# Kernel optimization log

Hardware: AMD Instinct MI355X
Metric: run time of the kernel (lower is better)

## Reference

```python
import jax, jax.numpy as jnp
import numpy as np

K = 256        # top-k positions kept along the sparse (sequence) axis
GROUPS = 16    # number of channel groups
P = 2          # Lp norm order
EPS = 1e-9


def setup_inputs() -> dict:
    key = jax.random.key(0)
    x = jax.random.normal(key, (32, 2048, 1024), dtype=jnp.float32)
    return {"x": x}


def reference(x):
    B, S, C = x.shape              # batch, sparse axis (seq), group axis (channels)
    g = GROUPS
    gs = C // g                    # channels per group
    # group-wise Lp norm: (B, S, g)
    xg = x.reshape(B, S, g, gs)
    norms = jnp.power(jnp.sum(jnp.power(jnp.abs(xg), P), axis=-1) + EPS, 1.0 / P)
    # topk along the sparse axis per (batch, group)
    norms_t = norms.transpose(0, 2, 1).reshape(B * g, S)   # (B*g, S)
    _, idx = jax.lax.top_k(norms_t, K)                      # (B*g, K)
    # scatter binary mask at topk positions
    rows = jnp.arange(B * g, dtype=jnp.int32)[:, None]
    mask = jnp.zeros((B * g, S), dtype=x.dtype).at[rows, idx].set(1.0)
    mask = mask.reshape(B, g, S).transpose(0, 2, 1)         # (B, S, g)
    # broadcast mask over channels within each group and multiply
    out = (mask[:, :, :, None] * xg).reshape(B, S, C)
    return out
```

## Files before the change

### kernel.cpp

```cpp
#include <hip/hip_runtime.h>


#define BB 32
#define SS 2048
#define GG 16
#define KTOP 256

typedef float f32x4 __attribute__((ext_vector_type(4)));

__device__ inline double shfl_xor_dbl(double v, int m) {
  union {
    double d;
    int i[2];
  } u;
  u.d = v;
  u.i[0] = __shfl_xor(u.i[0], m, 64);
  u.i[1] = __shfl_xor(u.i[1], m, 64);
  return u.d;
}

__global__ __launch_bounds__(1024, 8) void gsa_fused3(
    const float4* __restrict__ x4, float4* __restrict__ out4) {
  __shared__ float norm[SS];
  __shared__ unsigned int Tch_sh;
  __shared__ int Tscl_sh;
  const int t = threadIdx.x;
  const int lane16 = t & 15;
  const int srow = t >> 4;
  const int b = blockIdx.x >> 4;
  const int g = blockIdx.x & 15;
  const size_t bbase = (size_t)b * SS;
  const int chunk = g * 16 + lane16;

  for (int it = 0; it < 16; ++it) {
    const int s0 = it * 128 + srow;
    const int s1 = s0 + 64;
    const float4 va = x4[(bbase + s0) * 256 + chunk];
    const float4 vb = x4[(bbase + s1) * 256 + chunk];
    double da = (double)va.x * va.x + (double)va.y * va.y +
                (double)va.z * va.z + (double)va.w * va.w;
    double db = (double)vb.x * vb.x + (double)vb.y * vb.y +
                (double)vb.z * vb.z + (double)vb.w * vb.w;
    da += shfl_xor_dbl(da, 1);
    db += shfl_xor_dbl(db, 1);
    da += shfl_xor_dbl(da, 2);
    db += shfl_xor_dbl(db, 2);
    da += shfl_xor_dbl(da, 4);
    db += shfl_xor_dbl(db, 4);
    da += shfl_xor_dbl(da, 8);
    db += shfl_xor_dbl(db, 8);
    if (lane16 == 0) {
      norm[s0] = sqrtf(__fadd_rn((float)da, 1e-9f));
      norm[s1] = sqrtf(__fadd_rn((float)db, 1e-9f));
    }
  }
  __syncthreads();

  if (t < 64) {
    unsigned int nb[32];
#pragma unroll
    for (int j = 0; j < 32; ++j) nb[j] = __float_as_uint(norm[j * 64 + t]);
    unsigned long long T = 0ULL;
    for (int bit = 41; bit >= 0; --bit) {
      const unsigned long long cand = T | (1ULL << bit);
      const unsigned int ch = (unsigned int)(cand >> 11);
      const int scl = 2047 - (int)(cand & 2047ULL);
      int cnt = 0;
#pragma unroll
      for (int j = 0; j < 32; ++j) {
        const bool pred =
            (nb[j] > ch) | ((nb[j] == ch) & ((t + j * 64) <= scl));
        cnt += (int)__popcll(__ballot(pred));
      }
      if (cnt >= KTOP) T = cand;
    }
    if (t == 0) {
      Tch_sh = (unsigned int)(T >> 11);
      Tscl_sh = 2047 - (int)(T & 2047ULL);
    }
  }
  __syncthreads();
  const unsigned int ch = Tch_sh;
  const int scl = Tscl_sh;

  for (int it = 0; it < 16; ++it) {
    const int s0 = it * 128 + srow;
    const int s1 = s0 + 64;
    const unsigned int n0 = __float_as_uint(norm[s0]);
    const unsigned int n1 = __float_as_uint(norm[s1]);
    const bool sel0 = (n0 > ch) | ((n0 == ch) & (s0 <= scl));
    const bool sel1 = (n1 > ch) | ((n1 == ch) & (s1 <= scl));
    float4 v0 = make_float4(0.f, 0.f, 0.f, 0.f);
    float4 v1 = make_float4(0.f, 0.f, 0.f, 0.f);
    if (sel0) v0 = x4[(bbase + s0) * 256 + chunk];
    if (sel1) v1 = x4[(bbase + s1) * 256 + chunk];
    __builtin_nontemporal_store(*(const f32x4*)&v0,
                                (f32x4*)(out4 + (bbase + s0) * 256 + chunk));
    __builtin_nontemporal_store(*(const f32x4*)&v1,
                                (f32x4*)(out4 + (bbase + s1) * 256 + chunk));
  }
}

extern "C" void kernel_launch(void* const* d_in, const int* in_sizes, int n_in,
                              void* d_out, int out_size, void* d_ws,
                              size_t ws_size, hipStream_t stream) {
  const float4* x4 = (const float4*)d_in[0];
  float4* out4 = (float4*)d_out;
  gsa_fused3<<<BB * GG, 1024, 0, stream>>>(x4, out4);
}
```

Baseline: 473.5 us.

## Remap blocks for L2 reuse, halve block size, use plain stores

Blocks are reordered so that consecutive block IDs cover 8 batches and the same group, rather than all 16 groups of one batch. This changes which blocks run together and whether re-reads of x hit in cache. Block size drops from 1024 to 512 threads with 4 loads in flight per thread in the norm pass. The nontemporal stores become ordinary stores, which may let output writes pollute L2 and evict x before the second pass re-reads it.

After: 504.4 us. 1.07x slower.

```diff
diff --git a/kernel.cpp b/kernel.cpp
--- a/kernel.cpp
+++ b/kernel.cpp
@@ -5,8 +5,6 @@
 #define SS 2048
 #define GG 16
 #define KTOP 256
-
-typedef float f32x4 __attribute__((ext_vector_type(4)));
 
 __device__ inline double shfl_xor_dbl(double v, int m) {
   union {
@@ -19,39 +17,39 @@
   return u.d;
 }
 
-__global__ __launch_bounds__(1024, 8) void gsa_fused3(
-    const float4* __restrict__ x4, float4* __restrict__ out4) {
+__global__ __launch_bounds__(512, 4) void gsa_v4(const float4* __restrict__ x4,
+                                                 float4* __restrict__ out4) {
   __shared__ float norm[SS];
   __shared__ unsigned int Tch_sh;
   __shared__ int Tscl_sh;
   const int t = threadIdx.x;
   const int lane16 = t & 15;
   const int srow = t >> 4;
-  const int b = blockIdx.x >> 4;
-  const int g = blockIdx.x & 15;
+  const int n = blockIdx.x;
+  const int g = (n >> 3) & 15;
+  const int b = ((n >> 7) << 3) | (n & 7);
   const size_t bbase = (size_t)b * SS;
   const int chunk = g * 16 + lane16;
 
   for (int it = 0; it < 16; ++it) {
-    const int s0 = it * 128 + srow;
-    const int s1 = s0 + 64;
-    const float4 va = x4[(bbase + s0) * 256 + chunk];
-    const float4 vb = x4[(bbase + s1) * 256 + chunk];
-    double da = (double)va.x * va.x + (double)va.y * va.y +
-                (double)va.z * va.z + (double)va.w * va.w;
-    double db = (double)vb.x * vb.x + (double)vb.y * vb.y +
-                (double)vb.z * vb.z + (double)vb.w * vb.w;
-    da += shfl_xor_dbl(da, 1);
-    db += shfl_xor_dbl(db, 1);
-    da += shfl_xor_dbl(da, 2);
-    db += shfl_xor_dbl(db, 2);
-    da += shfl_xor_dbl(da, 4);
-    db += shfl_xor_dbl(db, 4);
-    da += shfl_xor_dbl(da, 8);
-    db += shfl_xor_dbl(db, 8);
+    const int sb = it * 128 + srow;
+    float4 v[4];
+#pragma unroll
+    for (int j = 0; j < 4; ++j) v[j] = x4[(bbase + sb + j * 32) * 256 + chunk];
+    double d[4];
+#pragma unroll
+    for (int j = 0; j < 4; ++j)
+      d[j] = (double)v[j].x * v[j].x + (double)v[j].y * v[j].y +
+             (double)v[j].z * v[j].z + (double)v[j].w * v[j].w;
+#pragma unroll
+    for (int m = 1; m <= 8; m <<= 1) {
+#pragma unroll
+      for (int j = 0; j < 4; ++j) d[j] += shfl_xor_dbl(d[j], m);
+    }
     if (lane16 == 0) {
-      norm[s0] = sqrtf(__fadd_rn((float)da, 1e-9f));
-      norm[s1] = sqrtf(__fadd_rn((float)db, 1e-9f));
+#pragma unroll
+      for (int j = 0; j < 4; ++j)
+        norm[sb + j * 32] = sqrtf(__fadd_rn((float)d[j], 1e-9f));
     }
   }
   __syncthreads();
@@ -83,21 +81,13 @@
   const unsigned int ch = Tch_sh;
   const int scl = Tscl_sh;
 
-  for (int it = 0; it < 16; ++it) {
-    const int s0 = it * 128 + srow;
-    const int s1 = s0 + 64;
-    const unsigned int n0 = __float_as_uint(norm[s0]);
-    const unsigned int n1 = __float_as_uint(norm[s1]);
-    const bool sel0 = (n0 > ch) | ((n0 == ch) & (s0 <= scl));
-    const bool sel1 = (n1 > ch) | ((n1 == ch) & (s1 <= scl));
-    float4 v0 = make_float4(0.f, 0.f, 0.f, 0.f);
-    float4 v1 = make_float4(0.f, 0.f, 0.f, 0.f);
-    if (sel0) v0 = x4[(bbase + s0) * 256 + chunk];
-    if (sel1) v1 = x4[(bbase + s1) * 256 + chunk];
-    __builtin_nontemporal_store(*(const f32x4*)&v0,
-                                (f32x4*)(out4 + (bbase + s0) * 256 + chunk));
-    __builtin_nontemporal_store(*(const f32x4*)&v1,
-                                (f32x4*)(out4 + (bbase + s1) * 256 + chunk));
+  for (int it = 0; it < SS / 32; ++it) {
+    const int s = it * 32 + srow;
+    const unsigned int nbits = __float_as_uint(norm[s]);
+    const bool sel = (nbits > ch) | ((nbits == ch) & (s <= scl));
+    float4 v = make_float4(0.f, 0.f, 0.f, 0.f);
+    if (sel) v = x4[(bbase + s) * 256 + chunk];
+    out4[(bbase + s) * 256 + chunk] = v;
   }
 }
 
@@ -106,5 +96,5 @@
                               size_t ws_size, hipStream_t stream) {
   const float4* x4 = (const float4*)d_in[0];
   float4* out4 = (float4*)d_out;
-  gsa_fused3<<<BB * GG, 1024, 0, stream>>>(x4, out4);
+  gsa_v4<<<BB * GG, 512, 0, stream>>>(x4, out4);
 }
```
